# Kernel optimization log

Hardware: AMD Instinct MI355X
Metric: run time of the kernel (lower is better)

The kernel has to match this reference:

```python
import jax, jax.numpy as jnp
import numpy as np


def setup_inputs() -> dict:
    key = jax.random.key(0)
    N, C, E, S = 200000, 128, 3200000, 5000
    k0, k1, k2 = jax.random.split(key, 3)
    x = jax.random.normal(k0, (N, C), dtype=jnp.float32)
    edge_index = jax.random.randint(k1, (2, E), 0, N, dtype=jnp.int32)
    starts = (jnp.arange(S, dtype=jnp.int32) * (N // S))  # sorted sentence start offsets
    node1_indices = starts
    node2_indices = starts + 1
    sent_indices = starts + 2
    W = jax.random.normal(k2, (C, 1), dtype=jnp.float32) * 0.1
    b = jnp.zeros((1,), dtype=jnp.float32)
    return dict(x=x, edge_index=edge_index, node1_indices=node1_indices,
                node2_indices=node2_indices, sent_indices=sent_indices,
                W=W, b=b, alpha=4)


def _gcn_score(x, edge_index, W, b):
    # PyG GCNConv: h = xW; add self-loops; sym-normalized aggregation; + bias
    N = x.shape[0]
    h = x @ W  # [N, 1]
    row, col = edge_index[0], edge_index[1]
    ones = jnp.ones(row.shape[0], dtype=x.dtype)
    deg = jax.ops.segment_sum(ones, col, num_segments=N) + 1.0  # self-loop included
    dis = jax.lax.rsqrt(deg)
    norm = dis[row] * dis[col]
    agg = jax.ops.segment_sum(h[row] * norm[:, None], col, num_segments=N)
    out = agg + h * (dis * dis)[:, None]  # self-loop term, norm = 1/deg
    return (out + b).squeeze(-1)  # [N]


def reference(x, edge_index, node1_indices, node2_indices, sent_indices, W, b, alpha):
    N = x.shape[0]
    S = node1_indices.shape[0]
    score = _gcn_score(x, edge_index, W, b)  # [N]

    # per-sentence segment ids: segment i = [node1_indices[i], node1_indices[i+1])
    seg = jnp.searchsorted(node1_indices, jnp.arange(N, dtype=node1_indices.dtype), side='right') - 1
    seg = jnp.clip(seg, 0, S - 1)

    # numerically-stable per-segment softmax of scores
    m = jax.ops.segment_max(score, seg, num_segments=S)
    e = jnp.exp(score - m[seg])
    Z = jax.ops.segment_sum(e, seg, num_segments=S)
    p = e / Z[seg]  # normalized scores per sentence

    # cutoff = max(p) - alpha * std(p) per sentence (population std, as np.std)
    cnt = jax.ops.segment_sum(jnp.ones(N, dtype=p.dtype), seg, num_segments=S)
    pmax = jax.ops.segment_max(p, seg, num_segments=S)
    mean = jax.ops.segment_sum(p, seg, num_segments=S) / cnt
    var = jax.ops.segment_sum(p * p, seg, num_segments=S) / cnt - mean * mean
    std = jnp.sqrt(jnp.maximum(var, 0.0))
    cutoff = pmax - jnp.float32(alpha) * std
    keep = p >= cutoff[seg]

    # union with node1/node2/sent special nodes (always kept)
    keep = keep.at[node1_indices].set(True)
    keep = keep.at[node2_indices].set(True)
    keep = keep.at[sent_indices].set(True)

    # remap: position of each kept node in the compacted ordering
    pos = jnp.cumsum(keep.astype(jnp.int32)) - 1  # valid only where keep

    # gated node features (masked-dense form of x[perm] * tanh(score[perm]))
    x_out = jnp.where(keep[:, None], x * jnp.tanh(score)[:, None], 0.0)

    new_node1 = pos[node1_indices]
    new_node2 = pos[node2_indices]
    new_sent = pos[sent_indices]

    # filter_adj: keep edges with both endpoints kept, remap endpoints
    row, col = edge_index[0], edge_index[1]
    edge_keep = keep[row] & keep[col]
    new_edge_index = jnp.where(edge_keep[None, :], pos[edge_index], -1)

    return (x_out, new_edge_index, keep, edge_keep, new_node1, new_node2, new_sent)
```

## Files before the change

kernel.cpp:

```cpp
#include <hip/hip_runtime.h>
#include <math.h>

#define FXSCALE 4398046511104.0
#define WINDOW 1984
#define NBMAX 128
#define BINB 2048
#define LDSCAP 12288

typedef float vfloat4 __attribute__((ext_vector_type(4)));

__global__ void k_hist(const int* __restrict__ ecol, int* __restrict__ binCnt,
                       int E, int NB) {
    __shared__ int cnt[NBMAX];
    int tid = threadIdx.x;
    for (int i = tid; i < NBMAX; i += 256) cnt[i] = 0;
    __syncthreads();
    for (long e = (long)blockIdx.x * 256 + tid; e < E; e += 512L * 256)
        atomicAdd(&cnt[ecol[e] / WINDOW], 1);
    __syncthreads();
    for (int i = tid; i < NB; i += 256)
        if (cnt[i] > 0) atomicAdd(&binCnt[i], cnt[i]);
}

__global__ void k_bin_h(const int* __restrict__ erow, const int* __restrict__ ecol,
                        const int* __restrict__ binCnt, int* __restrict__ binWr0,
                        int* __restrict__ binnedRow,
                        unsigned short* __restrict__ binnedCol16,
                        const float* __restrict__ x, const float* __restrict__ W,
                        double* __restrict__ h,
                        int E, int NB, int N, int C, int nBatches) {
    int blk = blockIdx.x;
    if (blk >= nBatches) {
        int t = (blk - nBatches) * 256 + threadIdx.x;
        int row = t >> 5;
        int lane = t & 31;
        if (row >= N) return;
        const float4* xr = (const float4*)(x + (size_t)row * C);
        const float4* w4 = (const float4*)W;
        int C4 = C >> 2;
        double acc = 0.0;
        for (int c = lane; c < C4; c += 32) {
            float4 xv = xr[c];
            float4 wv = w4[c];
            acc += (double)xv.x * (double)wv.x + (double)xv.y * (double)wv.y
                 + (double)xv.z * (double)wv.z + (double)xv.w * (double)wv.w;
        }
        #pragma unroll
        for (int o = 16; o > 0; o >>= 1) acc += __shfl_xor(acc, o);
        if (lane == 0) h[row] = acc;
        return;
    }
    __shared__ int cnt[NBMAX];
    __shared__ int bcS[NBMAX];
    __shared__ int lbase[NBMAX];
    __shared__ int gbase[NBMAX];
    __shared__ int lrow[BINB];
    __shared__ unsigned short lcol[BINB];
    __shared__ unsigned char lbin[BINB];
    int tid = threadIdx.x;
    for (int i = tid; i < NBMAX; i += 256) { cnt[i] = 0; bcS[i] = (i < NB) ? binCnt[i] : 0; }
    __syncthreads();
    long b0 = (long)blk * BINB;
    int n = (int)((E - b0) < (long)BINB ? (E - b0) : (long)BINB);
    int bA[8], rkA[8], rwA[8];
    unsigned short clA[8];
    #pragma unroll
    for (int k = 0; k < 8; k++) bA[k] = -1;
    int base_i = tid * 8;
    if (base_i + 8 <= n) {
        long e = b0 + base_i;
        int4 r0 = *(const int4*)(erow + e), r1 = *(const int4*)(erow + e + 4);
        int4 c0 = *(const int4*)(ecol + e), c1 = *(const int4*)(ecol + e + 4);
        int rr[8] = {r0.x, r0.y, r0.z, r0.w, r1.x, r1.y, r1.z, r1.w};
        int cc[8] = {c0.x, c0.y, c0.z, c0.w, c1.x, c1.y, c1.z, c1.w};
        #pragma unroll
        for (int k = 0; k < 8; k++) {
            int c = cc[k];
            int bb = c / WINDOW;
            bA[k] = bb; rwA[k] = rr[k]; clA[k] = (unsigned short)(c - bb * WINDOW);
            rkA[k] = atomicAdd(&cnt[bb], 1);
        }
    } else {
        for (int k = 0; k < 8; k++) {
            int i = base_i + k;
            if (i < n) {
                long e = b0 + i;
                int c = ecol[e];
                int bb = c / WINDOW;
                bA[k] = bb; rwA[k] = erow[e]; clA[k] = (unsigned short)(c - bb * WINDOW);
                rkA[k] = atomicAdd(&cnt[bb], 1);
            }
        }
    }
    __syncthreads();
    if (tid == 0) {
        int acc = 0;
        #pragma unroll 1
        for (int i = 0; i < NB; i++) { lbase[i] = acc; acc += cnt[i]; }
    }
    __syncthreads();
    if (tid < NB && cnt[tid] > 0) {
        int boff = 0;
        for (int i = 0; i < tid; i++) boff += bcS[i];
        gbase[tid] = boff + atomicAdd(&binWr0[tid], cnt[tid]);
    }
    __syncthreads();
    #pragma unroll
    for (int k = 0; k < 8; k++) {
        if (bA[k] >= 0) {
            int l = lbase[bA[k]] + rkA[k];
            lrow[l] = rwA[k];
            lcol[l] = clA[k];
            lbin[l] = (unsigned char)bA[k];
        }
    }
    __syncthreads();
    for (int l = tid; l < n; l += 256) {
        int bb = lbin[l];
        int g = gbase[bb] + (l - lbase[bb]);
        binnedRow[g] = lrow[l];
        binnedCol16[g] = lcol[l];
    }
}

__global__ void k_degb(const unsigned short* __restrict__ binnedCol16,
                       const int* __restrict__ binCnt,
                       unsigned int* __restrict__ partialDeg, int N, int Md, int NB) {
    __shared__ unsigned int cnt[WINDOW];
    __shared__ int bcS[NBMAX];
    __shared__ int boff[2];
    int bin = blockIdx.x / Md, m = blockIdx.x % Md;
    int tid = threadIdx.x;
    for (int i = tid; i < NB; i += 256) bcS[i] = binCnt[i];
    for (int i = tid; i < WINDOW; i += 256) cnt[i] = 0;
    __syncthreads();
    if (tid == 0) {
        int acc = 0;
        for (int i = 0; i < bin; i++) acc += bcS[i];
        boff[0] = acc;
        boff[1] = acc + bcS[bin];
    }
    __syncthreads();
    int st = boff[0], en = boff[1];
    for (int idx = st + m * 256 + tid; idx < en; idx += Md * 256)
        atomicAdd(&cnt[binnedCol16[idx]], 1u);
    __syncthreads();
    int wb = bin * WINDOW;
    int wlim = (N - wb) < WINDOW ? (N - wb) : WINDOW;
    for (int i = tid; i < wlim; i += 256)
        partialDeg[(size_t)m * N + wb + i] = cnt[i];
}

__global__ void k_dis_hd(const unsigned int* __restrict__ partialDeg,
                         const double* __restrict__ h,
                         double* __restrict__ dis, double* __restrict__ hd,
                         int N, int Md) {
    int i = blockIdx.x * blockDim.x + threadIdx.x;
    if (i >= N) return;
    unsigned int dsum = 0;
    for (int m = 0; m < Md; m++) dsum += partialDeg[(size_t)m * N + i];
    double d = 1.0 / sqrt((double)dsum + 1.0);
    dis[i] = d;
    hd[i] = h[i] * d;
}

__global__ void k_aggb(const int* __restrict__ binnedRow,
                       const unsigned short* __restrict__ binnedCol16,
                       const int* __restrict__ binCnt,
                       const double* __restrict__ hd, const double* __restrict__ dis,
                       unsigned long long* __restrict__ partialAgg, int N, int Ma, int NB) {
    __shared__ unsigned long long acc[WINDOW];
    __shared__ int bcS[NBMAX];
    __shared__ int boff[2];
    int bin = blockIdx.x / Ma, m = blockIdx.x % Ma;
    int tid = threadIdx.x;
    for (int i = tid; i < NB; i += 256) bcS[i] = binCnt[i];
    for (int i = tid; i < WINDOW; i += 256) acc[i] = 0ULL;
    __syncthreads();
    if (tid == 0) {
        int a = 0;
        for (int i = 0; i < bin; i++) a += bcS[i];
        boff[0] = a;
        boff[1] = a + bcS[bin];
    }
    __syncthreads();
    int st = boff[0], en = boff[1];
    int wb = bin * WINDOW;
    for (int idx = st + m * 256 + tid; idx < en; idx += Ma * 256) {
        int r = binnedRow[idx];
        int c16 = binnedCol16[idx];
        long long q = __double2ll_rn(hd[r] * dis[wb + c16] * FXSCALE);
        atomicAdd(&acc[c16], (unsigned long long)q);
    }
    __syncthreads();
    int wlim = (N - wb) < WINDOW ? (N - wb) : WINDOW;
    for (int i = tid; i < wlim; i += 256)
        partialAgg[(size_t)m * N + wb + i] = acc[i];
}

__global__ void k_score(const unsigned long long* __restrict__ partialAgg,
                        const double* __restrict__ h, const double* __restrict__ dis,
                        const float* __restrict__ bptr,
                        float* __restrict__ score32, float* __restrict__ tg,
                        int N, int Ma) {
    int i = blockIdx.x * blockDim.x + threadIdx.x;
    if (i >= N) return;
    long long acc = 0;
    for (int m = 0; m < Ma; m++) acc += (long long)partialAgg[(size_t)m * N + i];
    double agg = (double)acc / FXSCALE;
    double d = dis[i];
    double sc = (agg + h[i] * (d * d)) + (double)bptr[0];
    score32[i] = (float)sc;
    tg[i] = (float)tanh(sc);
}

__global__ void k_seg_scan(const float* __restrict__ score32, const float* __restrict__ tg,
                           const int* __restrict__ starts, const int* __restrict__ alphaPtr,
                           const int* __restrict__ n1, const int* __restrict__ n2,
                           const int* __restrict__ sent,
                           unsigned long long* __restrict__ stArr,
                           float* __restrict__ p32, int* __restrict__ keepG,
                           float* __restrict__ posF, float* __restrict__ gate,
                           float* __restrict__ o_keep, int N, int S) {
    __shared__ float scoreS[LDSCAP];
    __shared__ float pS[LDSCAP];
    __shared__ int smc[256];
    __shared__ int exclSh;
    int tid = threadIdx.x;
    int b = blockIdx.x;
    int g0 = b * 256;
    int segs = S - g0; if (segs > 256) segs = 256;
    int st0 = starts[g0];
    int en0 = (g0 + 256 >= S) ? N : starts[g0 + 256];
    int len = en0 - st0;
    bool useLds = (len <= LDSCAP);

    int ai = alphaPtr[0];
    float alpha = (ai >= 0 && ai < 1000000) ? (float)ai : __int_as_float(ai);

    int myKept = 0;
    int myStL = 0, myEnL = 0;
    bool active = false;

    if (useLds) {
        for (int i = tid; i < len; i += 256) scoreS[i] = score32[st0 + i];
        __syncthreads();
        int g = g0 + tid;
        if (tid < segs) {
            int st = starts[g] - st0;
            int en = ((g == S - 1) ? N : starts[g + 1]) - st0;
            if (en > st) {
                active = true; myStL = st; myEnL = en;
                float m = -3.402823466e38f;
                for (int i = st; i < en; i++) m = fmaxf(m, scoreS[i]);
                float Z = 0.0f;
                for (int i = st; i < en; i++) {
                    float dm = __fsub_rn(scoreS[i], m);
                    float e = (float)exp((double)dm);
                    pS[i] = e;
                    Z = __fadd_rn(Z, e);
                }
                float sp = 0.0f, sq = 0.0f, pm = -3.402823466e38f;
                for (int i = st; i < en; i++) {
                    float p = __fdiv_rn(pS[i], Z);
                    pS[i] = p;
                    sp = __fadd_rn(sp, p);
                    sq = __fadd_rn(sq, __fmul_rn(p, p));
                    pm = fmaxf(pm, p);
                }
                float cnt_ = (float)(en - st);
                float mean = __fdiv_rn(sp, cnt_);
                float var = __fsub_rn(__fdiv_rn(sq, cnt_), __fmul_rn(mean, mean));
                float sd = sqrtf(fmaxf(var, 0.0f));
                float cutoff = __fsub_rn(pm, __fmul_rn(alpha, sd));
                for (int i = st; i < en; i++)
                    scoreS[i] = (pS[i] >= cutoff) ? 1.0f : 0.0f;
                scoreS[n1[g] - st0] = 1.0f;
                scoreS[n2[g] - st0] = 1.0f;
                scoreS[sent[g] - st0] = 1.0f;
                int c = 0;
                for (int i = st; i < en; i++) c += (scoreS[i] != 0.0f) ? 1 : 0;
                myKept = c;
            }
        }
    } else {
        int g = g0 + tid;
        if (tid < segs) {
            int st = starts[g];
            int en = (g == S - 1) ? N : starts[g + 1];
            if (en > st) {
                active = true; myStL = st - st0; myEnL = en - st0;
                float m = -3.402823466e38f;
                for (int i = st; i < en; i++) m = fmaxf(m, score32[i]);
                float Z = 0.0f;
                for (int i = st; i < en; i++) {
                    float dm = __fsub_rn(score32[i], m);
                    float e = (float)exp((double)dm);
                    p32[i] = e;
                    Z = __fadd_rn(Z, e);
                }
                float sp = 0.0f, sq = 0.0f, pm = -3.402823466e38f;
                for (int i = st; i < en; i++) {
                    float p = __fdiv_rn(p32[i], Z);
                    p32[i] = p;
                    sp = __fadd_rn(sp, p);
                    sq = __fadd_rn(sq, __fmul_rn(p, p));
                    pm = fmaxf(pm, p);
                }
                float cnt_ = (float)(en - st);
                float mean = __fdiv_rn(sp, cnt_);
                float var = __fsub_rn(__fdiv_rn(sq, cnt_), __fmul_rn(mean, mean));
                float sd = sqrtf(fmaxf(var, 0.0f));
                float cutoff = __fsub_rn(pm, __fmul_rn(alpha, sd));
                for (int i = st; i < en; i++) keepG[i] = (p32[i] >= cutoff) ? 1 : 0;
                keepG[n1[g]] = 1; keepG[n2[g]] = 1; keepG[sent[g]] = 1;
                int c = 0;
                for (int i = st; i < en; i++) c += keepG[i];
                myKept = c;
            }
        }
    }
    smc[tid] = myKept;
    __syncthreads();
    for (int off2 = 1; off2 < 256; off2 <<= 1) {
        int t = (tid >= off2) ? smc[tid - off2] : 0;
        __syncthreads();
        smc[tid] += t;
        __syncthreads();
    }
    int total = smc[255];
    if (tid == 0) {
        if (b == 0) {
            atomicExch(&stArr[0], (2ULL << 62) | (unsigned long long)(unsigned)total);
            exclSh = 0;
        } else {
            atomicExch(&stArr[b], (1ULL << 62) | (unsigned long long)(unsigned)total);
            int excl = 0;
            int j = b - 1;
            while (true) {
                unsigned long long s = atomicAdd(&stArr[j], 0ULL);
                unsigned state = (unsigned)(s >> 62);
                if (state == 0) continue;
                excl += (int)(s & 0x3FFFFFFFFFFFFFFFULL);
                if (state == 2u) break;
                j--;
            }
            atomicExch(&stArr[b], (2ULL << 62) | (unsigned long long)(unsigned)(excl + total));
            exclSh = excl;
        }
    }
    __syncthreads();
    if (active) {
        int run = exclSh + smc[tid] - myKept;
        if (useLds) {
            for (int i = myStL; i < myEnL; i++) {
                if (scoreS[i] != 0.0f) { pS[i] = (float)run; run++; }
                else pS[i] = -1.0f;
            }
        } else {
            for (int i = myStL; i < myEnL; i++) {
                if (keepG[st0 + i]) { p32[st0 + i] = (float)run; run++; }
                else p32[st0 + i] = -1.0f;
            }
        }
    }
    __syncthreads();
    for (int i = tid; i < len; i += 256) {
        float pv = useLds ? pS[i] : p32[st0 + i];
        bool v = (pv >= 0.0f);
        posF[st0 + i] = pv;
        o_keep[st0 + i] = v ? 1.0f : 0.0f;
        gate[st0 + i] = v ? tg[st0 + i] : 0.0f;
    }
}

__global__ void k_out(const float4* __restrict__ x4, const float* __restrict__ gate,
                      float* __restrict__ o_x, long total4,
                      const int* __restrict__ erow, const int* __restrict__ ecol,
                      const float* __restrict__ posF,
                      float* __restrict__ o_edge, float* __restrict__ o_ekeep, int E,
                      const int* __restrict__ n1, const int* __restrict__ n2,
                      const int* __restrict__ sent,
                      float* __restrict__ o_n1, float* __restrict__ o_n2,
                      float* __restrict__ o_sent, int S,
                      int nxb, int neb4) {
    int b = blockIdx.x;
    if (b < nxb) {
        long idx = (long)b * blockDim.x + threadIdx.x;
        if (idx >= total4) return;
        int row = (int)(idx >> 5);
        float g = gate[row];
        float4 v = x4[idx];
        vfloat4 r = { v.x * g, v.y * g, v.z * g, v.w * g };
        __builtin_nontemporal_store(r, (vfloat4*)o_x + idx);
    } else if (b < nxb + neb4) {
        long e0 = ((long)(b - nxb) * blockDim.x + threadIdx.x) * 4;
        if (e0 >= E) return;
        if (e0 + 3 < E) {
            int4 r4 = *(const int4*)(erow + e0);
            int4 c4 = *(const int4*)(ecol + e0);
            vfloat4 oer, oec, ok;
            #pragma unroll
            for (int k = 0; k < 4; k++) {
                int r = (&r4.x)[k], c = (&c4.x)[k];
                float pr = posF[r], pc = posF[c];
                bool ek = (pr >= 0.0f) && (pc >= 0.0f);
                oer[k] = ek ? pr : -1.0f;
                oec[k] = ek ? pc : -1.0f;
                ok[k]  = ek ? 1.0f : 0.0f;
            }
            __builtin_nontemporal_store(oer, (vfloat4*)(o_edge + e0));
            __builtin_nontemporal_store(oec, (vfloat4*)(o_edge + (size_t)E + e0));
            __builtin_nontemporal_store(ok,  (vfloat4*)(o_ekeep + e0));
        } else {
            for (long e = e0; e < E; e++) {
                int r = erow[e], c = ecol[e];
                float pr = posF[r], pc = posF[c];
                bool ek = (pr >= 0.0f) && (pc >= 0.0f);
                o_edge[e] = ek ? pr : -1.0f;
                o_edge[(size_t)E + e] = ek ? pc : -1.0f;
                o_ekeep[e] = ek ? 1.0f : 0.0f;
            }
        }
    } else {
        int i = (b - nxb - neb4) * blockDim.x + threadIdx.x;
        if (i >= S) return;
        o_n1[i] = posF[n1[i]];
        o_n2[i] = posF[n2[i]];
        o_sent[i] = posF[sent[i]];
    }
}

extern "C" void kernel_launch(void* const* d_in, const int* in_sizes, int n_in,
                              void* d_out, int out_size, void* d_ws, size_t ws_size,
                              hipStream_t stream) {
    const float* x    = (const float*)d_in[0];
    const int*   eidx = (const int*)d_in[1];
    const int*   n1   = (const int*)d_in[2];
    const int*   n2   = (const int*)d_in[3];
    const int*   sent = (const int*)d_in[4];
    const float* W    = (const float*)d_in[5];
    const float* bp   = (const float*)d_in[6];
    const int*   alphaPtr = (const int*)d_in[7];

    int C = in_sizes[5];
    int N = in_sizes[0] / C;
    int E = in_sizes[1] / 2;
    int S = in_sizes[2];

    const int* erow = eidx;
    const int* ecol = eidx + E;

    int NB = (N + WINDOW - 1) / WINDOW;
    const int Md = 8, Ma = 8;
    int nsegb = (S + 255) / 256;
    int stN = nsegb > 256 ? nsegb : 256;

    char* ws = (char*)d_ws;
    size_t off = 0;
    auto alloc = [&](size_t bytes) { void* p = ws + off; off += (bytes + 255) & ~(size_t)255; return p; };
    int*   binCnt = (int*)  alloc(NBMAX * 4);
    int*   binWr0 = (int*)  alloc(NBMAX * 4);
    unsigned long long* scanSt = (unsigned long long*)alloc((size_t)stN * 8);
    size_t zeroBytes = (size_t)((char*)(scanSt + stN) - (char*)binCnt);
    int*   binnedRow = (int*)alloc((size_t)E * 4);
    unsigned short* binnedCol16 = (unsigned short*)alloc((size_t)E * 2);
    unsigned int* partialDeg = (unsigned int*)alloc((size_t)Md * N * 4);
    unsigned long long* partialAgg = (unsigned long long*)alloc((size_t)Ma * N * 8);
    double* h     = (double*)alloc((size_t)N * 8);
    double* dis   = (double*)alloc((size_t)N * 8);
    double* hd    = (double*)alloc((size_t)N * 8);
    float* score32 = (float*)alloc((size_t)N * 4);
    float* p32    = (float*)alloc((size_t)N * 4);
    float* tg     = (float*)alloc((size_t)N * 4);
    int*   keepG  = (int*)  alloc((size_t)N * 4);
    float* posF   = (float*)alloc((size_t)N * 4);
    float* gate   = (float*)alloc((size_t)N * 4);

    float* o_x     = (float*)d_out;
    float* o_edge  = o_x + (size_t)N * C;
    float* o_keep  = o_edge + 2 * (size_t)E;
    float* o_ekeep = o_keep + N;
    float* o_n1    = o_ekeep + E;
    float* o_n2    = o_n1 + S;
    float* o_sent  = o_n2 + S;

    (void)hipMemsetAsync(binCnt, 0, zeroBytes, stream);

    k_hist<<<512, 256, 0, stream>>>(ecol, binCnt, E, NB);
    int nBatches = (int)(((long)E + BINB - 1) / BINB);
    int nhb = (N * 32 + 255) / 256;
    k_bin_h<<<nBatches + nhb, 256, 0, stream>>>(erow, ecol, binCnt, binWr0,
                                                binnedRow, binnedCol16,
                                                x, W, h, E, NB, N, C, nBatches);
    k_degb<<<NB * Md, 256, 0, stream>>>(binnedCol16, binCnt, partialDeg, N, Md, NB);
    k_dis_hd<<<(N + 255) / 256, 256, 0, stream>>>(partialDeg, h, dis, hd, N, Md);
    k_aggb<<<NB * Ma, 256, 0, stream>>>(binnedRow, binnedCol16, binCnt, hd, dis, partialAgg, N, Ma, NB);
    k_score<<<(N + 255) / 256, 256, 0, stream>>>(partialAgg, h, dis, bp, score32, tg, N, Ma);
    k_seg_scan<<<nsegb, 256, 0, stream>>>(score32, tg, n1, alphaPtr, n1, n2, sent,
                                          scanSt, p32, keepG, posF, gate, o_keep, N, S);

    long total4 = (long)N * (C / 4);
    int nxb = (int)((total4 + 255) / 256);
    long e4 = (E + 3) / 4;
    int neb4 = (int)((e4 + 255) / 256);
    int nsb = (S + 255) / 256;
    k_out<<<nxb + neb4 + nsb, 256, 0, stream>>>(
        (const float4*)x, gate, o_x, total4,
        erow, ecol, posF, o_edge, o_ekeep, E,
        n1, n2, sent, o_n1, o_n2, o_sent, S, nxb, neb4);
}
```

Baseline: 232.9 us.

## Fuse degree/dis and aggregation/score kernels into one block per bin

Merges the per-bin degree count with the rsqrt/hd computation, and the per-bin aggregation with the final score/tanh step, using a single block per bin instead of eight partial blocks. This removes the partial-sum buffers, their global writes and reduction passes, and two kernel launches. The cost is much lower parallelism: only about one hundred blocks process all edges, which underfills the GPU.

```diff
diff --git a/kernel.cpp b/kernel.cpp
--- a/kernel.cpp
+++ b/kernel.cpp
@@ -123,13 +123,15 @@
     }
 }
 
-__global__ void k_degb(const unsigned short* __restrict__ binnedCol16,
-                       const int* __restrict__ binCnt,
-                       unsigned int* __restrict__ partialDeg, int N, int Md, int NB) {
+__global__ void k_deg_dis(const unsigned short* __restrict__ binnedCol16,
+                          const int* __restrict__ binCnt,
+                          const double* __restrict__ h,
+                          double* __restrict__ dis, double* __restrict__ hd,
+                          int N, int NB) {
     __shared__ unsigned int cnt[WINDOW];
     __shared__ int bcS[NBMAX];
     __shared__ int boff[2];
-    int bin = blockIdx.x / Md, m = blockIdx.x % Md;
+    int bin = blockIdx.x;
     int tid = threadIdx.x;
     for (int i = tid; i < NB; i += 256) bcS[i] = binCnt[i];
     for (int i = tid; i < WINDOW; i += 256) cnt[i] = 0;
@@ -142,37 +144,29 @@
     }
     __syncthreads();
     int st = boff[0], en = boff[1];
-    for (int idx = st + m * 256 + tid; idx < en; idx += Md * 256)
+    for (int idx = st + tid; idx < en; idx += 256)
         atomicAdd(&cnt[binnedCol16[idx]], 1u);
     __syncthreads();
     int wb = bin * WINDOW;
     int wlim = (N - wb) < WINDOW ? (N - wb) : WINDOW;
-    for (int i = tid; i < wlim; i += 256)
-        partialDeg[(size_t)m * N + wb + i] = cnt[i];
-}
-
-__global__ void k_dis_hd(const unsigned int* __restrict__ partialDeg,
-                         const double* __restrict__ h,
-                         double* __restrict__ dis, double* __restrict__ hd,
-                         int N, int Md) {
-    int i = blockIdx.x * blockDim.x + threadIdx.x;
-    if (i >= N) return;
-    unsigned int dsum = 0;
-    for (int m = 0; m < Md; m++) dsum += partialDeg[(size_t)m * N + i];
-    double d = 1.0 / sqrt((double)dsum + 1.0);
-    dis[i] = d;
-    hd[i] = h[i] * d;
-}
-
-__global__ void k_aggb(const int* __restrict__ binnedRow,
-                       const unsigned short* __restrict__ binnedCol16,
-                       const int* __restrict__ binCnt,
-                       const double* __restrict__ hd, const double* __restrict__ dis,
-                       unsigned long long* __restrict__ partialAgg, int N, int Ma, int NB) {
+    for (int i = tid; i < wlim; i += 256) {
+        double d = 1.0 / sqrt((double)cnt[i] + 1.0);
+        dis[wb + i] = d;
+        hd[wb + i] = h[wb + i] * d;
+    }
+}
+
+__global__ void k_agg_score(const int* __restrict__ binnedRow,
+                            const unsigned short* __restrict__ binnedCol16,
+                            const int* __restrict__ binCnt,
+                            const double* __restrict__ hd, const double* __restrict__ dis,
+                            const double* __restrict__ h, const float* __restrict__ bptr,
+                            float* __restrict__ score32, float* __restrict__ tg,
+                            int N, int NB) {
     __shared__ unsigned long long acc[WINDOW];
     __shared__ int bcS[NBMAX];
     __shared__ int boff[2];
-    int bin = blockIdx.x / Ma, m = blockIdx.x % Ma;
+    int bin = blockIdx.x;
     int tid = threadIdx.x;
     for (int i = tid; i < NB; i += 256) bcS[i] = binCnt[i];
     for (int i = tid; i < WINDOW; i += 256) acc[i] = 0ULL;
@@ -186,7 +180,7 @@
     __syncthreads();
     int st = boff[0], en = boff[1];
     int wb = bin * WINDOW;
-    for (int idx = st + m * 256 + tid; idx < en; idx += Ma * 256) {
+    for (int idx = st + tid; idx < en; idx += 256) {
         int r = binnedRow[idx];
         int c16 = binnedCol16[idx];
         long long q = __double2ll_rn(hd[r] * dis[wb + c16] * FXSCALE);
@@ -194,24 +188,14 @@
     }
     __syncthreads();
     int wlim = (N - wb) < WINDOW ? (N - wb) : WINDOW;
-    for (int i = tid; i < wlim; i += 256)
-        partialAgg[(size_t)m * N + wb + i] = acc[i];
-}
-
-__global__ void k_score(const unsigned long long* __restrict__ partialAgg,
-                        const double* __restrict__ h, const double* __restrict__ dis,
-                        const float* __restrict__ bptr,
-                        float* __restrict__ score32, float* __restrict__ tg,
-                        int N, int Ma) {
-    int i = blockIdx.x * blockDim.x + threadIdx.x;
-    if (i >= N) return;
-    long long acc = 0;
-    for (int m = 0; m < Ma; m++) acc += (long long)partialAgg[(size_t)m * N + i];
-    double agg = (double)acc / FXSCALE;
-    double d = dis[i];
-    double sc = (agg + h[i] * (d * d)) + (double)bptr[0];
-    score32[i] = (float)sc;
-    tg[i] = (float)tanh(sc);
+    double bb = (double)bptr[0];
+    for (int i = tid; i < wlim; i += 256) {
+        double agg = (double)(long long)acc[i] / FXSCALE;
+        double d = dis[wb + i];
+        double sc = (agg + h[wb + i] * (d * d)) + bb;
+        score32[wb + i] = (float)sc;
+        tg[wb + i] = (float)tanh(sc);
+    }
 }
 
 __global__ void k_seg_scan(const float* __restrict__ score32, const float* __restrict__ tg,
@@ -452,7 +436,6 @@
     const int* ecol = eidx + E;
 
     int NB = (N + WINDOW - 1) / WINDOW;
-    const int Md = 8, Ma = 8;
     int nsegb = (S + 255) / 256;
     int stN = nsegb > 256 ? nsegb : 256;
 
@@ -465,8 +448,6 @@
     size_t zeroBytes = (size_t)((char*)(scanSt + stN) - (char*)binCnt);
     int*   binnedRow = (int*)alloc((size_t)E * 4);
     unsigned short* binnedCol16 = (unsigned short*)alloc((size_t)E * 2);
-    unsigned int* partialDeg = (unsigned int*)alloc((size_t)Md * N * 4);
-    unsigned long long* partialAgg = (unsigned long long*)alloc((size_t)Ma * N * 8);
     double* h     = (double*)alloc((size_t)N * 8);
     double* dis   = (double*)alloc((size_t)N * 8);
     double* hd    = (double*)alloc((size_t)N * 8);
@@ -493,10 +474,9 @@
     k_bin_h<<<nBatches + nhb, 256, 0, stream>>>(erow, ecol, binCnt, binWr0,
                                                 binnedRow, binnedCol16,
                                                 x, W, h, E, NB, N, C, nBatches);
-    k_degb<<<NB * Md, 256, 0, stream>>>(binnedCol16, binCnt, partialDeg, N, Md, NB);
-    k_dis_hd<<<(N + 255) / 256, 256, 0, stream>>>(partialDeg, h, dis, hd, N, Md);
-    k_aggb<<<NB * Ma, 256, 0, stream>>>(binnedRow, binnedCol16, binCnt, hd, dis, partialAgg, N, Ma, NB);
-    k_score<<<(N + 255) / 256, 256, 0, stream>>>(partialAgg, h, dis, bp, score32, tg, N, Ma);
+    k_deg_dis<<<NB, 256, 0, stream>>>(binnedCol16, binCnt, h, dis, hd, N, NB);
+    k_agg_score<<<NB, 256, 0, stream>>>(binnedRow, binnedCol16, binCnt, hd, dis, h, bp,
+                                        score32, tg, N, NB);
     k_seg_scan<<<nsegb, 256, 0, stream>>>(score32, tg, n1, alphaPtr, n1, n2, sent,
                                           scanSt, p32, keepG, posF, gate, o_keep, N, S);
 
```

Result: slower. 282.3 us (+21.2%).

## Fuse score computation into segment scan and shrink segments per block

Applied to the files above, without the earlier changes.

Removes the separate k_score kernel. The segment-softmax kernel now reduces partialAgg and computes the score and tanh inline, keeping them in LDS, which drops the score32/tg global round trip and one launch. Segments per block go from 256 to 64 and the LDS capacity shrinks to match, so the grid grows from about 20 blocks to about 79 for more parallelism. The cost is that only 64 of 256 threads do the serial per-segment work, and the non-LDS fallback recomputes scores several times.

```diff
diff --git a/kernel.cpp b/kernel.cpp
--- a/kernel.cpp
+++ b/kernel.cpp
@@ -5,7 +5,8 @@
 #define WINDOW 1984
 #define NBMAX 128
 #define BINB 2048
-#define LDSCAP 12288
+#define SEGB 64
+#define LDSCAP 4096
 
 typedef float vfloat4 __attribute__((ext_vector_type(4)));
 
@@ -198,52 +199,52 @@
         partialAgg[(size_t)m * N + wb + i] = acc[i];
 }
 
-__global__ void k_score(const unsigned long long* __restrict__ partialAgg,
-                        const double* __restrict__ h, const double* __restrict__ dis,
-                        const float* __restrict__ bptr,
-                        float* __restrict__ score32, float* __restrict__ tg,
-                        int N, int Ma) {
-    int i = blockIdx.x * blockDim.x + threadIdx.x;
-    if (i >= N) return;
-    long long acc = 0;
-    for (int m = 0; m < Ma; m++) acc += (long long)partialAgg[(size_t)m * N + i];
-    double agg = (double)acc / FXSCALE;
-    double d = dis[i];
-    double sc = (agg + h[i] * (d * d)) + (double)bptr[0];
-    score32[i] = (float)sc;
-    tg[i] = (float)tanh(sc);
-}
-
-__global__ void k_seg_scan(const float* __restrict__ score32, const float* __restrict__ tg,
+__global__ void k_seg_scan(const unsigned long long* __restrict__ partialAgg,
+                           const double* __restrict__ h, const double* __restrict__ dis,
+                           const float* __restrict__ bptr,
                            const int* __restrict__ starts, const int* __restrict__ alphaPtr,
                            const int* __restrict__ n1, const int* __restrict__ n2,
                            const int* __restrict__ sent,
                            unsigned long long* __restrict__ stArr,
                            float* __restrict__ p32, int* __restrict__ keepG,
                            float* __restrict__ posF, float* __restrict__ gate,
-                           float* __restrict__ o_keep, int N, int S) {
+                           float* __restrict__ o_keep, int N, int S, int Ma) {
     __shared__ float scoreS[LDSCAP];
+    __shared__ float tgS[LDSCAP];
     __shared__ float pS[LDSCAP];
     __shared__ int smc[256];
     __shared__ int exclSh;
     int tid = threadIdx.x;
     int b = blockIdx.x;
-    int g0 = b * 256;
-    int segs = S - g0; if (segs > 256) segs = 256;
+    int g0 = b * SEGB;
+    int segs = S - g0; if (segs > SEGB) segs = SEGB;
     int st0 = starts[g0];
-    int en0 = (g0 + 256 >= S) ? N : starts[g0 + 256];
+    int en0 = (g0 + SEGB >= S) ? N : starts[g0 + SEGB];
     int len = en0 - st0;
     bool useLds = (len <= LDSCAP);
 
+    double bb = (double)bptr[0];
     int ai = alphaPtr[0];
     float alpha = (ai >= 0 && ai < 1000000) ? (float)ai : __int_as_float(ai);
+
+    auto scoreAtD = [&](int i) -> double {
+        long long acc = 0;
+        for (int m = 0; m < Ma; m++) acc += (long long)partialAgg[(size_t)m * N + i];
+        double agg = (double)acc / FXSCALE;
+        double d = dis[i];
+        return (agg + h[i] * (d * d)) + bb;
+    };
 
     int myKept = 0;
     int myStL = 0, myEnL = 0;
     bool active = false;
 
     if (useLds) {
-        for (int i = tid; i < len; i += 256) scoreS[i] = score32[st0 + i];
+        for (int i = tid; i < len; i += 256) {
+            double sc = scoreAtD(st0 + i);
+            scoreS[i] = (float)sc;
+            tgS[i] = (float)tanh(sc);
+        }
         __syncthreads();
         int g = g0 + tid;
         if (tid < segs) {
@@ -291,10 +292,10 @@
             if (en > st) {
                 active = true; myStL = st - st0; myEnL = en - st0;
                 float m = -3.402823466e38f;
-                for (int i = st; i < en; i++) m = fmaxf(m, score32[i]);
+                for (int i = st; i < en; i++) m = fmaxf(m, (float)scoreAtD(i));
                 float Z = 0.0f;
                 for (int i = st; i < en; i++) {
-                    float dm = __fsub_rn(score32[i], m);
+                    float dm = __fsub_rn((float)scoreAtD(i), m);
                     float e = (float)exp((double)dm);
                     p32[i] = e;
                     Z = __fadd_rn(Z, e);
@@ -370,7 +371,8 @@
         bool v = (pv >= 0.0f);
         posF[st0 + i] = pv;
         o_keep[st0 + i] = v ? 1.0f : 0.0f;
-        gate[st0 + i] = v ? tg[st0 + i] : 0.0f;
+        float tgv = useLds ? tgS[i] : (float)tanh(scoreAtD(st0 + i));
+        gate[st0 + i] = v ? tgv : 0.0f;
     }
 }
 
@@ -453,7 +455,7 @@
 
     int NB = (N + WINDOW - 1) / WINDOW;
     const int Md = 8, Ma = 8;
-    int nsegb = (S + 255) / 256;
+    int nsegb = (S + SEGB - 1) / SEGB;
     int stN = nsegb > 256 ? nsegb : 256;
 
     char* ws = (char*)d_ws;
@@ -470,9 +472,7 @@
     double* h     = (double*)alloc((size_t)N * 8);
     double* dis   = (double*)alloc((size_t)N * 8);
     double* hd    = (double*)alloc((size_t)N * 8);
-    float* score32 = (float*)alloc((size_t)N * 4);
     float* p32    = (float*)alloc((size_t)N * 4);
-    float* tg     = (float*)alloc((size_t)N * 4);
     int*   keepG  = (int*)  alloc((size_t)N * 4);
     float* posF   = (float*)alloc((size_t)N * 4);
     float* gate   = (float*)alloc((size_t)N * 4);
@@ -496,9 +496,8 @@
     k_degb<<<NB * Md, 256, 0, stream>>>(binnedCol16, binCnt, partialDeg, N, Md, NB);
     k_dis_hd<<<(N + 255) / 256, 256, 0, stream>>>(partialDeg, h, dis, hd, N, Md);
     k_aggb<<<NB * Ma, 256, 0, stream>>>(binnedRow, binnedCol16, binCnt, hd, dis, partialAgg, N, Ma, NB);
-    k_score<<<(N + 255) / 256, 256, 0, stream>>>(partialAgg, h, dis, bp, score32, tg, N, Ma);
-    k_seg_scan<<<nsegb, 256, 0, stream>>>(score32, tg, n1, alphaPtr, n1, n2, sent,
-                                          scanSt, p32, keepG, posF, gate, o_keep, N, S);
+    k_seg_scan<<<nsegb, 256, 0, stream>>>(partialAgg, h, dis, bp, n1, alphaPtr, n1, n2, sent,
+                                          scanSt, p32, keepG, posF, gate, o_keep, N, S, Ma);
 
     long total4 = (long)N * (C / 4);
     int nxb = (int)((total4 + 255) / 256);
```

Measured after the change: 240.8 us. +3.4%, slower.
